# Performance work log

Hardware: AMD Instinct MI355X
Metric: run time of the kernel (lower is better)

Reference implementation:

```python
import jax, jax.numpy as jnp
import numpy as np

KS_LIST = (7, 9, 11)
DILS = (1, 2, 4, 8, 16, 32)
PER = 5          # kernels per (kernel_size, dilation) group
EPS = 1e-5       # BatchNorm1d eps
N, C, L = 512, 12, 8192


def _rocket_features(x, W7, b7, W9, b9, W11, b11):
    # x: [N, C, L]; W_ks: [6*PER, C, ks]; b_ks: [6*PER]
    dn = ('NCH', 'OIH', 'NCH')
    feats = []
    for W, b in ((W7, b7), (W9, b9), (W11, b11)):
        for j, d in enumerate(DILS):
            w = W[j * PER:(j + 1) * PER]      # [PER, C, ks]
            bb = b[j * PER:(j + 1) * PER]     # [PER]
            # one dilated conv for all PER kernels in this group -> [N, PER, L]
            out = jax.lax.conv_general_dilated(
                x, w, window_strides=(1,), padding='SAME',
                rhs_dilation=(d,), dimension_numbers=dn) + bb[None, :, None]
            ppv = jnp.mean((out > 0).astype(x.dtype), axis=2)  # [N, PER]
            mx = jnp.max(out, axis=2)                          # [N, PER]
            # interleave (ppv_k, max_k) per kernel, matching the torch loop order
            feats.append(jnp.stack([ppv, mx], axis=-1).reshape(x.shape[0], 2 * PER))
    f = jnp.concatenate(feats, axis=1)  # [N, 2*nb_kernels] = [N, 180]
    # BatchNorm1d(affine=False), training mode: batch stats, biased variance
    mean = jnp.mean(f, axis=0)
    var = jnp.var(f, axis=0)
    return (f - mean) / jnp.sqrt(var + EPS)


def setup_inputs() -> dict:
    key = jax.random.key(0)
    kx, k1, k2, k3, k4, k5, k6 = jax.random.split(key, 7)
    G = len(DILS) * PER  # 30 kernels per kernel-size family
    inp = {
        'x': jax.random.normal(kx, (N, C, L), dtype=jnp.float32),
        'W7': jax.random.uniform(k1, (G, C, 7), minval=-1.0, maxval=1.0, dtype=jnp.float32),
        'b7': jax.random.normal(k2, (G,), dtype=jnp.float32),
        'W9': jax.random.uniform(k3, (G, C, 9), minval=-1.0, maxval=1.0, dtype=jnp.float32),
        'b9': jax.random.normal(k4, (G,), dtype=jnp.float32),
        'W11': jax.random.uniform(k5, (G, C, 11), minval=-1.0, maxval=1.0, dtype=jnp.float32),
        'b11': jax.random.normal(k6, (G,), dtype=jnp.float32),
    }
    return inp


def reference(x, W7, b7, W9, b9, W11, b11):
    return _rocket_features(x, W7, b7, W9, b9, W11, b11)
```

## Files before the change

### kernel.cpp

```cpp
#include <hip/hip_runtime.h>
#include <math.h>
#include <limits.h>

#define N_SAMP 512
#define C_IN   12
#define L_IN   8192
#define NDIL   6
#define NFILT  30
#define NFEAT  180
#define NCHUNK 4
#define CHUNK  (L_IN / NCHUNK)
#define EPSV   1e-5f

#define HALO   160
#define TLC    1024
#define LWC    (TLC + 2*HALO)
#define TILEB  (LWC * 16)
#define NST    (CHUNK / TLC)

#define WF_OFF (3 * N_SAMP * NCHUNK * NFILT * 2)
#define WTAB_B (NDIL * 3 * 64 * 16)

typedef __attribute__((ext_vector_type(4))) int i32x4;

__device__ __forceinline__ int swz(int r) {
    return (r << 4) ^ ((((r >> 3) ^ (r >> 6)) & 7) << 4);
}

__device__ __forceinline__ int imax(int a, int b) { return a > b ? a : b; }

__global__ __launch_bounds__(256)
void build_wb(const float* __restrict__ W7, const float* __restrict__ W9,
              const float* __restrict__ W11, const float* __restrict__ b7,
              const float* __restrict__ b9, const float* __restrict__ b11,
              signed char* __restrict__ wc, signed char* __restrict__ wd,
              float* __restrict__ bias_tab)
{
    const int t = blockIdx.x * 256 + threadIdx.x;
    if (t < NDIL * 3 * 64) {
        const int j    = t / 192;
        const int mf   = (t / 64) % 3;
        const int lane = t % 64;
        const int col  = lane & 15;
        const int q    = lane >> 4;
        const int tap  = mf * 4 + q;
#pragma unroll
        for (int e = 0; e < 16; ++e) {
            float v = 0.0f;
            if (col < 15 && tap <= 10 && e < 12) {
                const int toff = tap - 5;
                if (col < 5) {
                    if (toff >= -3 && toff <= 3)
                        v = W7[((j * 5 + col) * 12 + e) * 7 + toff + 3];
                } else if (col < 10) {
                    if (toff >= -4 && toff <= 4)
                        v = W9[((j * 5 + col - 5) * 12 + e) * 9 + toff + 4];
                } else {
                    v = W11[((j * 5 + col - 10) * 12 + e) * 11 + toff + 5];
                }
            }
            const int W  = __float2int_rn(v * 8192.0f);
            const int C8 = (W + 128) >> 8;
            const int D8 = W - (C8 << 8);
            wc[(size_t)t * 16 + e] = (signed char)C8;
            wd[(size_t)t * 16 + e] = (signed char)D8;
        }
    } else if (t < NDIL * 3 * 64 + 96) {
        const int i = t - NDIL * 3 * 64;
        const int j = i / 16, s = i % 16;
        float b = 0.0f;
        if (s < 5)       b = b7 [j * 5 + s];
        else if (s < 10) b = b9 [j * 5 + s - 5];
        else if (s < 15) b = b11[j * 5 + s - 10];
        bias_tab[j * 16 + s] = b;
    }
}

__global__ __launch_bounds__(256)
void rocket_conv_i8(const float* __restrict__ x,
                    const signed char* __restrict__ wc,
                    const signed char* __restrict__ wd,
                    const float* __restrict__ bias_tab,
                    float* __restrict__ ws)
{
    __shared__ __align__(16) signed char xq[2][TILEB];
    __shared__ int scnt[NDIL * 16];
    __shared__ int smx [NDIL * 16];

    const int ch  = blockIdx.x;
    const int n   = blockIdx.y;
    const int tid = threadIdx.x;
    const int lane = tid & 63, wv = tid >> 6;
    const int row_l = lane & 15, q = lane >> 4;
    const float* __restrict__ xrow = x + (size_t)n * C_IN * L_IN;
    const i32x4* __restrict__ wcv = (const i32x4*)wc;
    const i32x4* __restrict__ wdv = (const i32x4*)wd;

    if (tid < NDIL * 16) { scnt[tid] = 0; smx[tid] = INT_MIN; }

    const int c0 = ch * CHUNK;
#pragma unroll 1
    for (int st = 0; st < NST; ++st) {
        const int t0 = c0 + st * TLC;
        __syncthreads();
#pragma unroll 1
        for (int r = tid; r < LWC; r += 256) {
            const int g = t0 - HALO + r;
            int h[4] = {0, 0, 0, 0}, l[4] = {0, 0, 0, 0};
            if ((unsigned)g < (unsigned)L_IN) {
#pragma unroll
                for (int c = 0; c < 12; ++c) {
                    const float xv = xrow[c * L_IN + g];
                    const int X  = __float2int_rn(xv * 4096.0f);
                    const int A8 = (X + 128) >> 8;
                    const int B8 = X - (A8 << 8);
                    h[c >> 2] |= (A8 & 255) << ((c & 3) * 8);
                    l[c >> 2] |= (B8 & 255) << ((c & 3) * 8);
                }
            }
            const int cell = swz(r);
            *(i32x4*)&xq[0][cell] = (i32x4){h[0], h[1], h[2], h[3]};
            *(i32x4*)&xq[1][cell] = (i32x4){l[0], l[1], l[2], l[3]};
        }
        __syncthreads();

#pragma unroll 1
        for (int j = 0; j < NDIL; ++j) {
            const int d = 1 << j;
            const i32x4 C0 = wcv[(j * 3 + 0) * 64 + lane];
            const i32x4 C1 = wcv[(j * 3 + 1) * 64 + lane];
            const i32x4 C2 = wcv[(j * 3 + 2) * 64 + lane];
            const i32x4 D0 = wdv[(j * 3 + 0) * 64 + lane];
            const i32x4 D1 = wdv[(j * 3 + 1) * 64 + lane];
            const i32x4 D2 = wdv[(j * 3 + 2) * 64 + lane];
            const float bj = bias_tab[j * 16 + row_l];
            const int tj = (int)floorf(bj * -33554432.0f);
            const int r0 = HALO + wv * 256 + row_l + (q - 5) * d;
            const int r1 = HALO + wv * 256 + row_l + (q - 1) * d;
            const int r2 = HALO + wv * 256 + row_l +
                           ((q == 3) ? 0 : (q + 3) * d);

            int cnt_i = 0, mx_i = INT_MIN;
#pragma unroll 4
            for (int t = 0; t < 16; ++t) {
                const int cell0 = swz(r0 + 16 * t);
                const int cell1 = swz(r1 + 16 * t);
                const int cell2 = swz(r2 + 16 * t);
                i32x4 a0 = {0, 0, 0, 0};
                i32x4 a1 = {0, 0, 0, 0};
                i32x4 a2 = {0, 0, 0, 0};
                {
                    i32x4 ah = *(const i32x4*)&xq[0][cell0];
                    i32x4 al = *(const i32x4*)&xq[1][cell0];
                    a0 = __builtin_amdgcn_mfma_i32_16x16x64_i8(ah, C0, a0, 0, 0, 0);
                    a1 = __builtin_amdgcn_mfma_i32_16x16x64_i8(ah, D0, a1, 0, 0, 0);
                    a1 = __builtin_amdgcn_mfma_i32_16x16x64_i8(al, C0, a1, 0, 0, 0);
                    a2 = __builtin_amdgcn_mfma_i32_16x16x64_i8(al, D0, a2, 0, 0, 0);
                }
                {
                    i32x4 ah = *(const i32x4*)&xq[0][cell1];
                    i32x4 al = *(const i32x4*)&xq[1][cell1];
                    a0 = __builtin_amdgcn_mfma_i32_16x16x64_i8(ah, C1, a0, 0, 0, 0);
                    a1 = __builtin_amdgcn_mfma_i32_16x16x64_i8(ah, D1, a1, 0, 0, 0);
                    a1 = __builtin_amdgcn_mfma_i32_16x16x64_i8(al, C1, a1, 0, 0, 0);
                    a2 = __builtin_amdgcn_mfma_i32_16x16x64_i8(al, D1, a2, 0, 0, 0);
                }
                {
                    i32x4 ah = *(const i32x4*)&xq[0][cell2];
                    i32x4 al = *(const i32x4*)&xq[1][cell2];
                    a0 = __builtin_amdgcn_mfma_i32_16x16x64_i8(ah, C2, a0, 0, 0, 0);
                    a1 = __builtin_amdgcn_mfma_i32_16x16x64_i8(ah, D2, a1, 0, 0, 0);
                    a1 = __builtin_amdgcn_mfma_i32_16x16x64_i8(al, C2, a1, 0, 0, 0);
                    a2 = __builtin_amdgcn_mfma_i32_16x16x64_i8(al, D2, a2, 0, 0, 0);
                }
                const int v0 = ((a0[0] << 8) + a1[0] << 8) + a2[0];
                const int v1 = ((a0[1] << 8) + a1[1] << 8) + a2[1];
                const int v2 = ((a0[2] << 8) + a1[2] << 8) + a2[2];
                const int v3 = ((a0[3] << 8) + a1[3] << 8) + a2[3];
                cnt_i += (v0 > tj) + (v1 > tj) + (v2 > tj) + (v3 > tj);
                mx_i = imax(mx_i, imax(imax(v0, v1), imax(v2, v3)));
            }

            cnt_i += __shfl_xor(cnt_i, 16);
            cnt_i += __shfl_xor(cnt_i, 32);
            mx_i = imax(mx_i, __shfl_xor(mx_i, 16));
            mx_i = imax(mx_i, __shfl_xor(mx_i, 32));
            if (lane < 16) {
                atomicAdd(&scnt[j * 16 + lane], cnt_i);
                atomicMax(&smx[j * 16 + lane], mx_i);
            }
        }
    }

    __syncthreads();
    if (tid < 96) {
        const int jj = tid >> 4, s = tid & 15;
        if (s < 15) {
            const int c = scnt[jj * 16 + s];
            const int m = smx[jj * 16 + s];
            const float bj = bias_tab[jj * 16 + s];
            const int ks = s / 5, f = s % 5;
            const int gg = jj * 5 + f;
            const size_t base =
                ((((size_t)ks * N_SAMP + n) * NCHUNK + ch) * NFILT + gg) * 2;
            ws[base]     = (float)c;
            ws[base + 1] = bj + (float)m * 2.9802322387695312e-8f;
        }
    }
}

__global__ __launch_bounds__(512)
void rocket_finish(const float* __restrict__ ws, float* __restrict__ out)
{
    const int i = blockIdx.x;
    const int t = threadIdx.x;

    const int ks = i / 60;
    const int r  = i % 60;
    const int g  = r >> 1;
    const int m  = r & 1;

    const size_t base =
        ((((size_t)ks * N_SAMP + t) * NCHUNK) * NFILT + g) * 2 + m;

    float v;
    if (m) {
        v = -INFINITY;
#pragma unroll
        for (int c = 0; c < NCHUNK; ++c)
            v = fmaxf(v, ws[base + (size_t)c * NFILT * 2]);
    } else {
        v = 0.0f;
#pragma unroll
        for (int c = 0; c < NCHUNK; ++c)
            v += ws[base + (size_t)c * NFILT * 2];
        v *= (1.0f / (float)L_IN);
    }

    float s  = v;
    float sq = v * v;
#pragma unroll
    for (int off = 32; off; off >>= 1) {
        s  += __shfl_xor(s, off);
        sq += __shfl_xor(sq, off);
    }

    __shared__ float ss[8], sqq[8];
    const int lane = t & 63;
    const int wv   = t >> 6;
    if (lane == 0) { ss[wv] = s; sqq[wv] = sq; }
    __syncthreads();
    if (t == 0) {
        float S = 0.0f, Q = 0.0f;
#pragma unroll
        for (int w = 0; w < 8; ++w) { S += ss[w]; Q += sqq[w]; }
        ss[0] = S; sqq[0] = Q;
    }
    __syncthreads();

    const float mean = ss[0] * (1.0f / (float)N_SAMP);
    const float var  = sqq[0] * (1.0f / (float)N_SAMP) - mean * mean;
    out[t * NFEAT + i] = (v - mean) / sqrtf(var + EPSV);
}

extern "C" void kernel_launch(void* const* d_in, const int* in_sizes, int n_in,
                              void* d_out, int out_size, void* d_ws, size_t ws_size,
                              hipStream_t stream)
{
    const float* x   = (const float*)d_in[0];
    const float* W7  = (const float*)d_in[1];
    const float* b7  = (const float*)d_in[2];
    const float* W9  = (const float*)d_in[3];
    const float* b9  = (const float*)d_in[4];
    const float* W11 = (const float*)d_in[5];
    const float* b11 = (const float*)d_in[6];
    float* out = (float*)d_out;
    float* ws  = (float*)d_ws;
    signed char* wc = (signed char*)(ws + WF_OFF);
    signed char* wd = wc + WTAB_B;
    float* bias_tab = (float*)(wd + WTAB_B);

    build_wb<<<5, 256, 0, stream>>>(W7, W9, W11, b7, b9, b11, wc, wd, bias_tab);

    dim3 grid(NCHUNK, N_SAMP);
    rocket_conv_i8<<<grid, 256, 0, stream>>>(x, wc, wd, bias_tab, ws);

    rocket_finish<<<NFEAT, 512, 0, stream>>>(ws, out);
}
```

Baseline: 273.2 us.

## Double block size, prefetch next-dilation weights, fold bias into MFMA accumulator

The conv kernel now launches 512 threads per block, so each of 8 waves handles 128 positions per tile instead of 256 and the tile loads are spread across more threads. Weight fragments for the next dilation are prefetched into registers while the current one computes, and the quantized bias seeds the low accumulator so the threshold compare becomes a compare against zero and the final bias add is dropped. s_setprio raises wave priority around the MFMA loop. In exchange, register pressure rises from the prefetched weights under a 512-thread launch bound, and rounding the bias to an integer slightly changes results versus the old floor-based threshold.

```diff
diff --git a/kernel.cpp b/kernel.cpp
--- a/kernel.cpp
+++ b/kernel.cpp
@@ -17,6 +17,7 @@
 #define LWC    (TLC + 2*HALO)
 #define TILEB  (LWC * 16)
 #define NST    (CHUNK / TLC)
+#define BLK    512
 
 #define WF_OFF (3 * N_SAMP * NCHUNK * NFILT * 2)
 #define WTAB_B (NDIL * 3 * 64 * 16)
@@ -76,7 +77,7 @@
     }
 }
 
-__global__ __launch_bounds__(256)
+__global__ __launch_bounds__(BLK)
 void rocket_conv_i8(const float* __restrict__ x,
                     const signed char* __restrict__ wc,
                     const signed char* __restrict__ wd,
@@ -104,7 +105,7 @@
         const int t0 = c0 + st * TLC;
         __syncthreads();
 #pragma unroll 1
-        for (int r = tid; r < LWC; r += 256) {
+        for (int r = tid; r < LWC; r += BLK) {
             const int g = t0 - HALO + r;
             int h[4] = {0, 0, 0, 0}, l[4] = {0, 0, 0, 0};
             if ((unsigned)g < (unsigned)L_IN) {
@@ -124,62 +125,73 @@
         }
         __syncthreads();
 
+        i32x4 cC0 = wcv[0 * 64 + lane];
+        i32x4 cC1 = wcv[1 * 64 + lane];
+        i32x4 cC2 = wcv[2 * 64 + lane];
+        i32x4 cD0 = wdv[0 * 64 + lane];
+        i32x4 cD1 = wdv[1 * 64 + lane];
+        i32x4 cD2 = wdv[2 * 64 + lane];
 #pragma unroll 1
         for (int j = 0; j < NDIL; ++j) {
             const int d = 1 << j;
-            const i32x4 C0 = wcv[(j * 3 + 0) * 64 + lane];
-            const i32x4 C1 = wcv[(j * 3 + 1) * 64 + lane];
-            const i32x4 C2 = wcv[(j * 3 + 2) * 64 + lane];
-            const i32x4 D0 = wdv[(j * 3 + 0) * 64 + lane];
-            const i32x4 D1 = wdv[(j * 3 + 1) * 64 + lane];
-            const i32x4 D2 = wdv[(j * 3 + 2) * 64 + lane];
+            i32x4 nC0, nC1, nC2, nD0, nD1, nD2;
+            if (j < NDIL - 1) {
+                nC0 = wcv[((j + 1) * 3 + 0) * 64 + lane];
+                nC1 = wcv[((j + 1) * 3 + 1) * 64 + lane];
+                nC2 = wcv[((j + 1) * 3 + 2) * 64 + lane];
+                nD0 = wdv[((j + 1) * 3 + 0) * 64 + lane];
+                nD1 = wdv[((j + 1) * 3 + 1) * 64 + lane];
+                nD2 = wdv[((j + 1) * 3 + 2) * 64 + lane];
+            }
             const float bj = bias_tab[j * 16 + row_l];
-            const int tj = (int)floorf(bj * -33554432.0f);
-            const int r0 = HALO + wv * 256 + row_l + (q - 5) * d;
-            const int r1 = HALO + wv * 256 + row_l + (q - 1) * d;
-            const int r2 = HALO + wv * 256 + row_l +
+            const int bias_i = __float2int_rn(bj * 33554432.0f);
+            const int r0 = HALO + wv * 128 + row_l + (q - 5) * d;
+            const int r1 = HALO + wv * 128 + row_l + (q - 1) * d;
+            const int r2 = HALO + wv * 128 + row_l +
                            ((q == 3) ? 0 : (q + 3) * d);
 
             int cnt_i = 0, mx_i = INT_MIN;
+            __builtin_amdgcn_s_setprio(1);
 #pragma unroll 4
-            for (int t = 0; t < 16; ++t) {
+            for (int t = 0; t < 8; ++t) {
                 const int cell0 = swz(r0 + 16 * t);
                 const int cell1 = swz(r1 + 16 * t);
                 const int cell2 = swz(r2 + 16 * t);
                 i32x4 a0 = {0, 0, 0, 0};
                 i32x4 a1 = {0, 0, 0, 0};
-                i32x4 a2 = {0, 0, 0, 0};
+                i32x4 a2 = {bias_i, bias_i, bias_i, bias_i};
                 {
                     i32x4 ah = *(const i32x4*)&xq[0][cell0];
                     i32x4 al = *(const i32x4*)&xq[1][cell0];
-                    a0 = __builtin_amdgcn_mfma_i32_16x16x64_i8(ah, C0, a0, 0, 0, 0);
-                    a1 = __builtin_amdgcn_mfma_i32_16x16x64_i8(ah, D0, a1, 0, 0, 0);
-                    a1 = __builtin_amdgcn_mfma_i32_16x16x64_i8(al, C0, a1, 0, 0, 0);
-                    a2 = __builtin_amdgcn_mfma_i32_16x16x64_i8(al, D0, a2, 0, 0, 0);
+                    a0 = __builtin_amdgcn_mfma_i32_16x16x64_i8(ah, cC0, a0, 0, 0, 0);
+                    a1 = __builtin_amdgcn_mfma_i32_16x16x64_i8(ah, cD0, a1, 0, 0, 0);
+                    a1 = __builtin_amdgcn_mfma_i32_16x16x64_i8(al, cC0, a1, 0, 0, 0);
+                    a2 = __builtin_amdgcn_mfma_i32_16x16x64_i8(al, cD0, a2, 0, 0, 0);
                 }
                 {
                     i32x4 ah = *(const i32x4*)&xq[0][cell1];
                     i32x4 al = *(const i32x4*)&xq[1][cell1];
-                    a0 = __builtin_amdgcn_mfma_i32_16x16x64_i8(ah, C1, a0, 0, 0, 0);
-                    a1 = __builtin_amdgcn_mfma_i32_16x16x64_i8(ah, D1, a1, 0, 0, 0);
-                    a1 = __builtin_amdgcn_mfma_i32_16x16x64_i8(al, C1, a1, 0, 0, 0);
-                    a2 = __builtin_amdgcn_mfma_i32_16x16x64_i8(al, D1, a2, 0, 0, 0);
+                    a0 = __builtin_amdgcn_mfma_i32_16x16x64_i8(ah, cC1, a0, 0, 0, 0);
+                    a1 = __builtin_amdgcn_mfma_i32_16x16x64_i8(ah, cD1, a1, 0, 0, 0);
+                    a1 = __builtin_amdgcn_mfma_i32_16x16x64_i8(al, cC1, a1, 0, 0, 0);
+                    a2 = __builtin_amdgcn_mfma_i32_16x16x64_i8(al, cD1, a2, 0, 0, 0);
                 }
                 {
                     i32x4 ah = *(const i32x4*)&xq[0][cell2];
                     i32x4 al = *(const i32x4*)&xq[1][cell2];
-                    a0 = __builtin_amdgcn_mfma_i32_16x16x64_i8(ah, C2, a0, 0, 0, 0);
-                    a1 = __builtin_amdgcn_mfma_i32_16x16x64_i8(ah, D2, a1, 0, 0, 0);
-                    a1 = __builtin_amdgcn_mfma_i32_16x16x64_i8(al, C2, a1, 0, 0, 0);
-                    a2 = __builtin_amdgcn_mfma_i32_16x16x64_i8(al, D2, a2, 0, 0, 0);
+                    a0 = __builtin_amdgcn_mfma_i32_16x16x64_i8(ah, cC2, a0, 0, 0, 0);
+                    a1 = __builtin_amdgcn_mfma_i32_16x16x64_i8(ah, cD2, a1, 0, 0, 0);
+                    a1 = __builtin_amdgcn_mfma_i32_16x16x64_i8(al, cC2, a1, 0, 0, 0);
+                    a2 = __builtin_amdgcn_mfma_i32_16x16x64_i8(al, cD2, a2, 0, 0, 0);
                 }
                 const int v0 = ((a0[0] << 8) + a1[0] << 8) + a2[0];
                 const int v1 = ((a0[1] << 8) + a1[1] << 8) + a2[1];
                 const int v2 = ((a0[2] << 8) + a1[2] << 8) + a2[2];
                 const int v3 = ((a0[3] << 8) + a1[3] << 8) + a2[3];
-                cnt_i += (v0 > tj) + (v1 > tj) + (v2 > tj) + (v3 > tj);
+                cnt_i += (v0 > 0) + (v1 > 0) + (v2 > 0) + (v3 > 0);
                 mx_i = imax(mx_i, imax(imax(v0, v1), imax(v2, v3)));
             }
+            __builtin_amdgcn_s_setprio(0);
 
             cnt_i += __shfl_xor(cnt_i, 16);
             cnt_i += __shfl_xor(cnt_i, 32);
@@ -189,6 +201,11 @@
                 atomicAdd(&scnt[j * 16 + lane], cnt_i);
                 atomicMax(&smx[j * 16 + lane], mx_i);
             }
+
+            if (j < NDIL - 1) {
+                cC0 = nC0; cC1 = nC1; cC2 = nC2;
+                cD0 = nD0; cD1 = nD1; cD2 = nD2;
+            }
         }
     }
 
@@ -198,13 +215,12 @@
         if (s < 15) {
             const int c = scnt[jj * 16 + s];
             const int m = smx[jj * 16 + s];
-            const float bj = bias_tab[jj * 16 + s];
             const int ks = s / 5, f = s % 5;
             const int gg = jj * 5 + f;
             const size_t base =
                 ((((size_t)ks * N_SAMP + n) * NCHUNK + ch) * NFILT + gg) * 2;
             ws[base]     = (float)c;
-            ws[base + 1] = bj + (float)m * 2.9802322387695312e-8f;
+            ws[base + 1] = (float)m * 2.9802322387695312e-8f;
         }
     }
 }
@@ -283,7 +299,7 @@
     build_wb<<<5, 256, 0, stream>>>(W7, W9, W11, b7, b9, b11, wc, wd, bias_tab);
 
     dim3 grid(NCHUNK, N_SAMP);
-    rocket_conv_i8<<<grid, 256, 0, stream>>>(x, wc, wd, bias_tab, ws);
+    rocket_conv_i8<<<grid, BLK, 0, stream>>>(x, wc, wd, bias_tab, ws);
 
     rocket_finish<<<NFEAT, 512, 0, stream>>>(ws, out);
 }
```

Result: slower. 306.6 us (+12.2%).
